# Kernel tuning notes

Hardware: AMD Instinct MI355X
Metric: run time of the kernel (lower is better)

Reference implementation:

```python
import jax, jax.numpy as jnp
import numpy as np

T, H, I, E, K = 1024, 2048, 768, 32, 4


def setup_inputs() -> dict:
    key = jax.random.key(0)
    ks = jax.random.split(key, 6)
    x = jax.random.normal(ks[0], (T, H), dtype=jnp.float32)
    # torch nn.Linear weight layout: [out_features, in_features], no bias (Qwen3)
    Wg = jax.random.normal(ks[1], (E, I, H), dtype=jnp.float32) * 0.02
    Wu = jax.random.normal(ks[2], (E, I, H), dtype=jnp.float32) * 0.02
    Wd = jax.random.normal(ks[3], (E, H, I), dtype=jnp.float32) * 0.02
    expert_ids = jax.random.randint(ks[4], (T, K), 0, E)
    expert_weights = jax.random.uniform(ks[5], (T, K), dtype=jnp.float32)
    return {"x": x, "Wg": Wg, "Wu": Wu, "Wd": Wd,
            "expert_ids": expert_ids, "expert_weights": expert_weights}


def reference(x, Wg, Wu, Wd, expert_ids, expert_weights):
    """MoE dispatch/combine over per-expert SwiGLU MLPs.

    y[t] = sum_k w[t,k] * down_e(silu(gate_e(x[t])) * up_e(x[t])), e = expert_ids[t,k]
    """
    Tn, Hn = x.shape
    En = Wg.shape[0]
    # Dense combine matrix [T, E]: scatter-add router weights onto expert slots.
    combine = jnp.zeros((Tn, En), x.dtype).at[
        jnp.arange(Tn)[:, None], expert_ids].add(expert_weights)

    def body(acc, we):
        wg, wu, wd, c = we  # wg,wu: [I,H]; wd: [H,I]; c: [T]
        h = jax.nn.silu(x @ wg.T) * (x @ wu.T)  # [T, I]
        return acc + c[:, None] * (h @ wd.T), None

    y, _ = jax.lax.scan(body, jnp.zeros_like(x), (Wg, Wu, Wd, combine.T))
    return y
```

## Files before the change

kernel.cpp:

```cpp
#include <hip/hip_runtime.h>
#include <hip/hip_bf16.h>

#define T_TOK 1024
#define H_DIM 2048
#define I_DIM 768
#define E_NUM 32
#define K_TOP 4
#define NPAIR (T_TOK * K_TOP)
#define TM 32
#define MAX_SLOTS (NPAIR + E_NUM * TM)

#define WS_META   0
#define WS_TOKEN  2048
#define WS_WEIGHT (WS_TOKEN + MAX_SLOTS * 4)
#define WS_HBUF   (WS_WEIGHT + MAX_SLOTS * 4)
#define WS_XB     (WS_HBUF + MAX_SLOTS * I_DIM * 2)

typedef __bf16 bf16x8 __attribute__((ext_vector_type(8)));
typedef float f32x4 __attribute__((ext_vector_type(4)));
typedef float f32x8 __attribute__((ext_vector_type(8)));

__device__ inline bf16x8 cvt8(f32x8 v) {
    bf16x8 r;
#pragma unroll
    for (int i = 0; i < 8; ++i) r[i] = (__bf16)v[i];
    return r;
}

__global__ void moe_route(const int* __restrict__ ids,
                          const float* __restrict__ ew,
                          int* __restrict__ meta,
                          int* __restrict__ slot_tok,
                          float* __restrict__ slot_w) {
    __shared__ int cnt[E_NUM], off[E_NUM], cur[E_NUM];
    __shared__ int s_tot;
    const int tid = threadIdx.x;
    if (tid < E_NUM) cnt[tid] = 0;
    __syncthreads();
    for (int p = tid; p < NPAIR; p += blockDim.x)
        atomicAdd(&cnt[ids[p]], 1);
    __syncthreads();
    if (tid == 0) {
        int tot = 0;
        for (int e = 0; e < E_NUM; ++e) {
            int pad = (cnt[e] + TM - 1) / TM * TM;
            off[e] = tot;
            meta[8 + e]  = tot;
            meta[64 + e] = pad / TM;
            tot += pad;
        }
        meta[0] = tot;
        s_tot = tot;
    }
    __syncthreads();
    const int tot = s_tot;
    for (int s = tid; s < tot; s += blockDim.x) {
        slot_tok[s] = 0;
        slot_w[s]   = 0.0f;
    }
    if (tid < E_NUM) cur[tid] = 0;
    __syncthreads();
    for (int p = tid; p < NPAIR; p += blockDim.x) {
        int e = ids[p];
        int i = atomicAdd(&cur[e], 1);
        int s = off[e] + i;
        slot_tok[s] = p / K_TOP;
        slot_w[s]   = ew[p];
    }
}

__global__ __launch_bounds__(256) void moe_xcast(const float* __restrict__ X,
                                                 __hip_bfloat16* __restrict__ Xb) {
    const int i = (blockIdx.x * 256 + threadIdx.x) * 8;
    f32x8 v = *(const f32x8*)(X + i);
    *(bf16x8*)(void*)(Xb + i) = cvt8(v);
}

template<int NMT>
__device__ __forceinline__ void gu_group(
    const __hip_bfloat16* __restrict__ Xb,
    const float* __restrict__ pg, const float* __restrict__ pu,
    const int* __restrict__ slot_tok,
    __hip_bfloat16* __restrict__ Hb,
    int off, int tile0, int n0, int col, int quad) {
    int s0[NMT];
    const __hip_bfloat16 *px0[NMT], *px1[NMT];
#pragma unroll
    for (int m = 0; m < NMT; ++m) {
        s0[m] = off + TM * (tile0 + 2 * m);
        px0[m] = Xb + (size_t)slot_tok[s0[m] + col] * H_DIM;
        px1[m] = Xb + (size_t)slot_tok[s0[m] + 16 + col] * H_DIM;
    }
    f32x4 ag0[NMT], ag1[NMT], au0[NMT], au1[NMT];
#pragma unroll
    for (int m = 0; m < NMT; ++m) {
        ag0[m] = {0.f,0.f,0.f,0.f}; ag1[m] = {0.f,0.f,0.f,0.f};
        au0[m] = {0.f,0.f,0.f,0.f}; au1[m] = {0.f,0.f,0.f,0.f};
    }
    for (int k = quad * 8; k < H_DIM; k += 32) {
        bf16x8 bg = cvt8(*(const f32x8*)(pg + k));
        bf16x8 bu = cvt8(*(const f32x8*)(pu + k));
#pragma unroll
        for (int m = 0; m < NMT; ++m) {
            bf16x8 a0 = *(const bf16x8*)(const void*)(px0[m] + k);
            bf16x8 a1 = *(const bf16x8*)(const void*)(px1[m] + k);
            ag0[m] = __builtin_amdgcn_mfma_f32_16x16x32_bf16(a0, bg, ag0[m], 0, 0, 0);
            ag1[m] = __builtin_amdgcn_mfma_f32_16x16x32_bf16(a1, bg, ag1[m], 0, 0, 0);
            au0[m] = __builtin_amdgcn_mfma_f32_16x16x32_bf16(a0, bu, au0[m], 0, 0, 0);
            au1[m] = __builtin_amdgcn_mfma_f32_16x16x32_bf16(a1, bu, au1[m], 0, 0, 0);
        }
    }
#pragma unroll
    for (int m = 0; m < NMT; ++m) {
#pragma unroll
        for (int r = 0; r < 4; ++r) {
            const int row = quad * 4 + r;
            float g0 = ag0[m][r], u0 = au0[m][r];
            float h0 = (g0 / (1.0f + __expf(-g0))) * u0;
            Hb[(size_t)(s0[m] + row) * I_DIM + n0 + col] = __float2bfloat16(h0);
            float g1 = ag1[m][r], u1 = au1[m][r];
            float h1 = (g1 / (1.0f + __expf(-g1))) * u1;
            Hb[(size_t)(s0[m] + 16 + row) * I_DIM + n0 + col] = __float2bfloat16(h1);
        }
    }
}

__global__ __launch_bounds__(256) void moe_gateup(
    const __hip_bfloat16* __restrict__ Xb,
    const float* __restrict__ Wg,
    const float* __restrict__ Wu,
    const int* __restrict__ meta,
    const int* __restrict__ slot_tok,
    __hip_bfloat16* __restrict__ Hb) {
    const int NCH = I_DIM / 32;
    const int e   = blockIdx.x / NCH;
    const int nch = blockIdx.x - e * NCH;
    const int lane = threadIdx.x & 63;
    const int wave = threadIdx.x >> 6;
    const int col  = lane & 15;
    const int quad = lane >> 4;
    const int colg = wave & 1;
    const int half = wave >> 1;
    const int n0 = nch * 32 + colg * 16;

    const int off   = meta[8 + e];
    const int ntile = meta[64 + e];
    const int nw = (ntile > half) ? ((ntile - half + 1) >> 1) : 0;
    if (nw == 0) return;

    const size_t wrow = ((size_t)e * I_DIM + n0 + col) * H_DIM;
    const float* pg = Wg + wrow;
    const float* pu = Wu + wrow;

    for (int i0 = 0; i0 < nw; i0 += 3) {
        int g = nw - i0; if (g > 3) g = 3;
        const int tile0 = half + 2 * i0;
        switch (g) {
            case 1:  gu_group<1>(Xb, pg, pu, slot_tok, Hb, off, tile0, n0, col, quad); break;
            case 2:  gu_group<2>(Xb, pg, pu, slot_tok, Hb, off, tile0, n0, col, quad); break;
            default: gu_group<3>(Xb, pg, pu, slot_tok, Hb, off, tile0, n0, col, quad); break;
        }
    }
}

template<int NMT>
__device__ __forceinline__ void dn_group(
    const float* __restrict__ pd,
    const int* __restrict__ slot_tok,
    const float* __restrict__ slot_w,
    const __hip_bfloat16* __restrict__ Hb,
    float* __restrict__ Y,
    int off, int tile0, int n0, int col, int quad) {
    int s0[NMT];
    const __hip_bfloat16 *ph0[NMT], *ph1[NMT];
#pragma unroll
    for (int m = 0; m < NMT; ++m) {
        s0[m] = off + TM * (tile0 + 2 * m);
        ph0[m] = Hb + (size_t)(s0[m] + col) * I_DIM;
        ph1[m] = Hb + (size_t)(s0[m] + 16 + col) * I_DIM;
    }
    f32x4 a0[NMT], a1[NMT];
#pragma unroll
    for (int m = 0; m < NMT; ++m) { a0[m] = {0.f,0.f,0.f,0.f}; a1[m] = {0.f,0.f,0.f,0.f}; }

    for (int k = quad * 8; k < I_DIM; k += 32) {
        bf16x8 b = cvt8(*(const f32x8*)(pd + k));
#pragma unroll
        for (int m = 0; m < NMT; ++m) {
            bf16x8 h0 = *(const bf16x8*)(const void*)(ph0[m] + k);
            bf16x8 h1 = *(const bf16x8*)(const void*)(ph1[m] + k);
            a0[m] = __builtin_amdgcn_mfma_f32_16x16x32_bf16(h0, b, a0[m], 0, 0, 0);
            a1[m] = __builtin_amdgcn_mfma_f32_16x16x32_bf16(h1, b, a1[m], 0, 0, 0);
        }
    }
#pragma unroll
    for (int m = 0; m < NMT; ++m) {
#pragma unroll
        for (int r = 0; r < 4; ++r) {
            const int row = quad * 4 + r;
            const int sA = s0[m] + row;
            atomicAdd(&Y[(size_t)slot_tok[sA] * H_DIM + n0 + col], a0[m][r] * slot_w[sA]);
            const int sB = s0[m] + 16 + row;
            atomicAdd(&Y[(size_t)slot_tok[sB] * H_DIM + n0 + col], a1[m][r] * slot_w[sB]);
        }
    }
}

__global__ __launch_bounds__(256) void moe_down(
    const float* __restrict__ Wd,
    const int* __restrict__ meta,
    const int* __restrict__ slot_tok,
    const float* __restrict__ slot_w,
    const __hip_bfloat16* __restrict__ Hb,
    float* __restrict__ Y) {
    const int NCH = H_DIM / 32;
    const int e   = blockIdx.x / NCH;
    const int nch = blockIdx.x - e * NCH;
    const int lane = threadIdx.x & 63;
    const int wave = threadIdx.x >> 6;
    const int col  = lane & 15;
    const int quad = lane >> 4;
    const int colg = wave & 1;
    const int half = wave >> 1;
    const int n0 = nch * 32 + colg * 16;

    const int off   = meta[8 + e];
    const int ntile = meta[64 + e];
    const int nw = (ntile > half) ? ((ntile - half + 1) >> 1) : 0;
    if (nw == 0) return;

    const float* pd = Wd + ((size_t)e * H_DIM + n0 + col) * I_DIM;

    for (int i0 = 0; i0 < nw; i0 += 3) {
        int g = nw - i0; if (g > 3) g = 3;
        const int tile0 = half + 2 * i0;
        switch (g) {
            case 1:  dn_group<1>(pd, slot_tok, slot_w, Hb, Y, off, tile0, n0, col, quad); break;
            case 2:  dn_group<2>(pd, slot_tok, slot_w, Hb, Y, off, tile0, n0, col, quad); break;
            default: dn_group<3>(pd, slot_tok, slot_w, Hb, Y, off, tile0, n0, col, quad); break;
        }
    }
}

extern "C" void kernel_launch(void* const* d_in, const int* in_sizes, int n_in,
                              void* d_out, int out_size, void* d_ws, size_t ws_size,
                              hipStream_t stream) {
    const float* X  = (const float*)d_in[0];
    const float* Wg = (const float*)d_in[1];
    const float* Wu = (const float*)d_in[2];
    const float* Wd = (const float*)d_in[3];
    const int* ids  = (const int*)d_in[4];
    const float* ew = (const float*)d_in[5];

    char* ws = (char*)d_ws;
    int*   meta     = (int*)(ws + WS_META);
    int*   slot_tok = (int*)(ws + WS_TOKEN);
    float* slot_w   = (float*)(ws + WS_WEIGHT);
    __hip_bfloat16* Hb = (__hip_bfloat16*)(ws + WS_HBUF);
    __hip_bfloat16* Xb = (__hip_bfloat16*)(ws + WS_XB);
    float* Y = (float*)d_out;

    hipMemsetAsync(Y, 0, (size_t)T_TOK * H_DIM * sizeof(float), stream);
    moe_route<<<1, 256, 0, stream>>>(ids, ew, meta, slot_tok, slot_w);
    moe_xcast<<<(T_TOK * H_DIM / 8) / 256, 256, 0, stream>>>(X, Xb);
    moe_gateup<<<E_NUM * (I_DIM / 32), 256, 0, stream>>>(Xb, Wg, Wu, meta, slot_tok, Hb);
    moe_down<<<E_NUM * (H_DIM / 32), 256, 0, stream>>>(Wd, meta, slot_tok, slot_w, Hb, Y);
}
```

Baseline: 810.5 us.

## Software-pipeline MFMA K-loops and give each block 16 columns across four waves

Both expert GEMM kernels now double-buffer their register loads: the next K-step's weight and activation vectors are fetched while MFMAs run on the current step. The block mapping also changes so each block covers 16 output columns with all four waves splitting tiles four ways, which doubles the grid and cuts the group size from three tiles to two. This is meant to hide global-load latency and raise parallelism. In exchange it uses more registers, and each block's column slice of the weights is now read by more waves.

```diff
diff --git a/kernel.cpp b/kernel.cpp
--- a/kernel.cpp
+++ b/kernel.cpp
@@ -87,7 +87,7 @@
     const __hip_bfloat16 *px0[NMT], *px1[NMT];
 #pragma unroll
     for (int m = 0; m < NMT; ++m) {
-        s0[m] = off + TM * (tile0 + 2 * m);
+        s0[m] = off + TM * (tile0 + 4 * m);
         px0[m] = Xb + (size_t)slot_tok[s0[m] + col] * H_DIM;
         px1[m] = Xb + (size_t)slot_tok[s0[m] + 16 + col] * H_DIM;
     }
@@ -97,19 +97,54 @@
         ag0[m] = {0.f,0.f,0.f,0.f}; ag1[m] = {0.f,0.f,0.f,0.f};
         au0[m] = {0.f,0.f,0.f,0.f}; au1[m] = {0.f,0.f,0.f,0.f};
     }
-    for (int k = quad * 8; k < H_DIM; k += 32) {
-        bf16x8 bg = cvt8(*(const f32x8*)(pg + k));
-        bf16x8 bu = cvt8(*(const f32x8*)(pu + k));
+    const int kq = quad * 8;
+    bf16x8 wg2[2], wu2[2];
+    bf16x8 a02[2][NMT], a12[2][NMT];
+    {
+        f32x8 g = *(const f32x8*)(pg + kq);
+        f32x8 u = *(const f32x8*)(pu + kq);
 #pragma unroll
         for (int m = 0; m < NMT; ++m) {
-            bf16x8 a0 = *(const bf16x8*)(const void*)(px0[m] + k);
-            bf16x8 a1 = *(const bf16x8*)(const void*)(px1[m] + k);
-            ag0[m] = __builtin_amdgcn_mfma_f32_16x16x32_bf16(a0, bg, ag0[m], 0, 0, 0);
-            ag1[m] = __builtin_amdgcn_mfma_f32_16x16x32_bf16(a1, bg, ag1[m], 0, 0, 0);
-            au0[m] = __builtin_amdgcn_mfma_f32_16x16x32_bf16(a0, bu, au0[m], 0, 0, 0);
-            au1[m] = __builtin_amdgcn_mfma_f32_16x16x32_bf16(a1, bu, au1[m], 0, 0, 0);
-        }
-    }
+            a02[0][m] = *(const bf16x8*)(const void*)(px0[m] + kq);
+            a12[0][m] = *(const bf16x8*)(const void*)(px1[m] + kq);
+        }
+        wg2[0] = cvt8(g); wu2[0] = cvt8(u);
+    }
+
+#define GU_STEP(CUR, IT) do {                                                  \
+        const int kn_ = kq + ((IT) + 1) * 32;                                  \
+        f32x8 g_ = *(const f32x8*)(pg + kn_);                                  \
+        f32x8 u_ = *(const f32x8*)(pu + kn_);                                  \
+        _Pragma("unroll")                                                      \
+        for (int m = 0; m < NMT; ++m) {                                        \
+            a02[1 - (CUR)][m] = *(const bf16x8*)(const void*)(px0[m] + kn_);   \
+            a12[1 - (CUR)][m] = *(const bf16x8*)(const void*)(px1[m] + kn_);   \
+        }                                                                      \
+        _Pragma("unroll")                                                      \
+        for (int m = 0; m < NMT; ++m) {                                        \
+            ag0[m] = __builtin_amdgcn_mfma_f32_16x16x32_bf16(a02[(CUR)][m], wg2[(CUR)], ag0[m], 0, 0, 0); \
+            ag1[m] = __builtin_amdgcn_mfma_f32_16x16x32_bf16(a12[(CUR)][m], wg2[(CUR)], ag1[m], 0, 0, 0); \
+            au0[m] = __builtin_amdgcn_mfma_f32_16x16x32_bf16(a02[(CUR)][m], wu2[(CUR)], au0[m], 0, 0, 0); \
+            au1[m] = __builtin_amdgcn_mfma_f32_16x16x32_bf16(a12[(CUR)][m], wu2[(CUR)], au1[m], 0, 0, 0); \
+        }                                                                      \
+        wg2[1 - (CUR)] = cvt8(g_); wu2[1 - (CUR)] = cvt8(u_);                  \
+    } while (0)
+
+    const int NIT = H_DIM / 32;
+    for (int it = 0; it < NIT - 2; it += 2) {
+        GU_STEP(0, it);
+        GU_STEP(1, it + 1);
+    }
+    GU_STEP(0, NIT - 2);
+#undef GU_STEP
+#pragma unroll
+    for (int m = 0; m < NMT; ++m) {
+        ag0[m] = __builtin_amdgcn_mfma_f32_16x16x32_bf16(a02[1][m], wg2[1], ag0[m], 0, 0, 0);
+        ag1[m] = __builtin_amdgcn_mfma_f32_16x16x32_bf16(a12[1][m], wg2[1], ag1[m], 0, 0, 0);
+        au0[m] = __builtin_amdgcn_mfma_f32_16x16x32_bf16(a02[1][m], wu2[1], au0[m], 0, 0, 0);
+        au1[m] = __builtin_amdgcn_mfma_f32_16x16x32_bf16(a12[1][m], wu2[1], au1[m], 0, 0, 0);
+    }
+
 #pragma unroll
     for (int m = 0; m < NMT; ++m) {
 #pragma unroll
@@ -132,34 +167,28 @@
     const int* __restrict__ meta,
     const int* __restrict__ slot_tok,
     __hip_bfloat16* __restrict__ Hb) {
-    const int NCH = I_DIM / 32;
+    const int NCH = I_DIM / 16;
     const int e   = blockIdx.x / NCH;
     const int nch = blockIdx.x - e * NCH;
     const int lane = threadIdx.x & 63;
     const int wave = threadIdx.x >> 6;
     const int col  = lane & 15;
     const int quad = lane >> 4;
-    const int colg = wave & 1;
-    const int half = wave >> 1;
-    const int n0 = nch * 32 + colg * 16;
+    const int n0 = nch * 16;
 
     const int off   = meta[8 + e];
     const int ntile = meta[64 + e];
-    const int nw = (ntile > half) ? ((ntile - half + 1) >> 1) : 0;
+    const int nw = (ntile > wave) ? ((ntile - wave + 3) >> 2) : 0;
     if (nw == 0) return;
 
     const size_t wrow = ((size_t)e * I_DIM + n0 + col) * H_DIM;
     const float* pg = Wg + wrow;
     const float* pu = Wu + wrow;
 
-    for (int i0 = 0; i0 < nw; i0 += 3) {
-        int g = nw - i0; if (g > 3) g = 3;
-        const int tile0 = half + 2 * i0;
-        switch (g) {
-            case 1:  gu_group<1>(Xb, pg, pu, slot_tok, Hb, off, tile0, n0, col, quad); break;
-            case 2:  gu_group<2>(Xb, pg, pu, slot_tok, Hb, off, tile0, n0, col, quad); break;
-            default: gu_group<3>(Xb, pg, pu, slot_tok, Hb, off, tile0, n0, col, quad); break;
-        }
+    for (int i0 = 0; i0 < nw; i0 += 2) {
+        const int tile0 = wave + 4 * i0;
+        if (nw - i0 >= 2) gu_group<2>(Xb, pg, pu, slot_tok, Hb, off, tile0, n0, col, quad);
+        else              gu_group<1>(Xb, pg, pu, slot_tok, Hb, off, tile0, n0, col, quad);
     }
 }
 
@@ -175,7 +204,7 @@
     const __hip_bfloat16 *ph0[NMT], *ph1[NMT];
 #pragma unroll
     for (int m = 0; m < NMT; ++m) {
-        s0[m] = off + TM * (tile0 + 2 * m);
+        s0[m] = off + TM * (tile0 + 4 * m);
         ph0[m] = Hb + (size_t)(s0[m] + col) * I_DIM;
         ph1[m] = Hb + (size_t)(s0[m] + 16 + col) * I_DIM;
     }
@@ -183,16 +212,48 @@
 #pragma unroll
     for (int m = 0; m < NMT; ++m) { a0[m] = {0.f,0.f,0.f,0.f}; a1[m] = {0.f,0.f,0.f,0.f}; }
 
-    for (int k = quad * 8; k < I_DIM; k += 32) {
-        bf16x8 b = cvt8(*(const f32x8*)(pd + k));
+    const int kq = quad * 8;
+    bf16x8 w2[2];
+    bf16x8 h02[2][NMT], h12[2][NMT];
+    {
+        f32x8 w = *(const f32x8*)(pd + kq);
 #pragma unroll
         for (int m = 0; m < NMT; ++m) {
-            bf16x8 h0 = *(const bf16x8*)(const void*)(ph0[m] + k);
-            bf16x8 h1 = *(const bf16x8*)(const void*)(ph1[m] + k);
-            a0[m] = __builtin_amdgcn_mfma_f32_16x16x32_bf16(h0, b, a0[m], 0, 0, 0);
-            a1[m] = __builtin_amdgcn_mfma_f32_16x16x32_bf16(h1, b, a1[m], 0, 0, 0);
-        }
-    }
+            h02[0][m] = *(const bf16x8*)(const void*)(ph0[m] + kq);
+            h12[0][m] = *(const bf16x8*)(const void*)(ph1[m] + kq);
+        }
+        w2[0] = cvt8(w);
+    }
+
+#define DN_STEP(CUR, IT) do {                                                  \
+        const int kn_ = kq + ((IT) + 1) * 32;                                  \
+        f32x8 w_ = *(const f32x8*)(pd + kn_);                                  \
+        _Pragma("unroll")                                                      \
+        for (int m = 0; m < NMT; ++m) {                                        \
+            h02[1 - (CUR)][m] = *(const bf16x8*)(const void*)(ph0[m] + kn_);   \
+            h12[1 - (CUR)][m] = *(const bf16x8*)(const void*)(ph1[m] + kn_);   \
+        }                                                                      \
+        _Pragma("unroll")                                                      \
+        for (int m = 0; m < NMT; ++m) {                                        \
+            a0[m] = __builtin_amdgcn_mfma_f32_16x16x32_bf16(h02[(CUR)][m], w2[(CUR)], a0[m], 0, 0, 0); \
+            a1[m] = __builtin_amdgcn_mfma_f32_16x16x32_bf16(h12[(CUR)][m], w2[(CUR)], a1[m], 0, 0, 0); \
+        }                                                                      \
+        w2[1 - (CUR)] = cvt8(w_);                                              \
+    } while (0)
+
+    const int NIT = I_DIM / 32;
+    for (int it = 0; it < NIT - 2; it += 2) {
+        DN_STEP(0, it);
+        DN_STEP(1, it + 1);
+    }
+    DN_STEP(0, NIT - 2);
+#undef DN_STEP
+#pragma unroll
+    for (int m = 0; m < NMT; ++m) {
+        a0[m] = __builtin_amdgcn_mfma_f32_16x16x32_bf16(h02[1][m], w2[1], a0[m], 0, 0, 0);
+        a1[m] = __builtin_amdgcn_mfma_f32_16x16x32_bf16(h12[1][m], w2[1], a1[m], 0, 0, 0);
+    }
+
 #pragma unroll
     for (int m = 0; m < NMT; ++m) {
 #pragma unroll
@@ -213,32 +274,26 @@
     const float* __restrict__ slot_w,
     const __hip_bfloat16* __restrict__ Hb,
     float* __restrict__ Y) {
-    const int NCH = H_DIM / 32;
+    const int NCH = H_DIM / 16;
     const int e   = blockIdx.x / NCH;
     const int nch = blockIdx.x - e * NCH;
     const int lane = threadIdx.x & 63;
     const int wave = threadIdx.x >> 6;
     const int col  = lane & 15;
     const int quad = lane >> 4;
-    const int colg = wave & 1;
-    const int half = wave >> 1;
-    const int n0 = nch * 32 + colg * 16;
+    const int n0 = nch * 16;
 
     const int off   = meta[8 + e];
     const int ntile = meta[64 + e];
-    const int nw = (ntile > half) ? ((ntile - half + 1) >> 1) : 0;
+    const int nw = (ntile > wave) ? ((ntile - wave + 3) >> 2) : 0;
     if (nw == 0) return;
 
     const float* pd = Wd + ((size_t)e * H_DIM + n0 + col) * I_DIM;
 
-    for (int i0 = 0; i0 < nw; i0 += 3) {
-        int g = nw - i0; if (g > 3) g = 3;
-        const int tile0 = half + 2 * i0;
-        switch (g) {
-            case 1:  dn_group<1>(pd, slot_tok, slot_w, Hb, Y, off, tile0, n0, col, quad); break;
-            case 2:  dn_group<2>(pd, slot_tok, slot_w, Hb, Y, off, tile0, n0, col, quad); break;
-            default: dn_group<3>(pd, slot_tok, slot_w, Hb, Y, off, tile0, n0, col, quad); break;
-        }
+    for (int i0 = 0; i0 < nw; i0 += 2) {
+        const int tile0 = wave + 4 * i0;
+        if (nw - i0 >= 2) dn_group<2>(pd, slot_tok, slot_w, Hb, Y, off, tile0, n0, col, quad);
+        else              dn_group<1>(pd, slot_tok, slot_w, Hb, Y, off, tile0, n0, col, quad);
     }
 }
 
@@ -263,6 +318,6 @@
     hipMemsetAsync(Y, 0, (size_t)T_TOK * H_DIM * sizeof(float), stream);
     moe_route<<<1, 256, 0, stream>>>(ids, ew, meta, slot_tok, slot_w);
     moe_xcast<<<(T_TOK * H_DIM / 8) / 256, 256, 0, stream>>>(X, Xb);
-    moe_gateup<<<E_NUM * (I_DIM / 32), 256, 0, stream>>>(Xb, Wg, Wu, meta, slot_tok, Hb);
-    moe_down<<<E_NUM * (H_DIM / 32), 256, 0, stream>>>(Wd, meta, slot_tok, slot_w, Hb, Y);
-}
+    moe_gateup<<<E_NUM * (I_DIM / 16), 256, 0, stream>>>(Xb, Wg, Wu, meta, slot_tok, Hb);
+    moe_down<<<E_NUM * (H_DIM / 16), 256, 0, stream>>>(Wd, meta, slot_tok, slot_w, Hb, Y);
+}
```

New measurement: 888.6 us. +9.6%, slower.

## Stage expert weight tiles in LDS with async double-buffered loads shared by all waves

Applied to the files above, without the earlier changes.

Gate/up and down kernels now give each block 16 output columns and have all four waves cooperatively stream fp32 weight tiles into swizzled, double-buffered LDS via global_load_lds. Each wave then handles up to two 32-row token tiles against the shared weight tile. Previously each wave read its own weight rows directly from global memory. This removes the redundant weight reads across waves and overlaps weight fetch with MFMA work. The cost is twice as many blocks, a barrier per k-step, and idle waves when an expert has few tiles.

```diff
diff --git a/kernel.cpp b/kernel.cpp
--- a/kernel.cpp
+++ b/kernel.cpp
@@ -20,11 +20,29 @@
 typedef float f32x4 __attribute__((ext_vector_type(4)));
 typedef float f32x8 __attribute__((ext_vector_type(8)));
 
+#define MFMA(acc, a, b) acc = __builtin_amdgcn_mfma_f32_16x16x32_bf16(a, b, acc, 0, 0, 0)
+
 __device__ inline bf16x8 cvt8(f32x8 v) {
     bf16x8 r;
 #pragma unroll
     for (int i = 0; i < 8; ++i) r[i] = (__bf16)v[i];
     return r;
+}
+
+__device__ __forceinline__ void stage16(const void* g, void* l) {
+    __builtin_amdgcn_global_load_lds(
+        (__attribute__((address_space(1))) void*)(void*)(size_t)g,
+        (__attribute__((address_space(3))) void*)l, 16, 0, 0);
+}
+
+__device__ __forceinline__ bf16x8 bfrag(const char* tile, int c, int jq) {
+    const int key = (c & 7) << 4;
+    f32x4 lo = *(const f32x4*)(tile + c * 256 + ((jq +  0) ^ key));
+    f32x4 hi = *(const f32x4*)(tile + c * 256 + ((jq + 16) ^ key));
+    f32x8 v;
+    v[0] = lo[0]; v[1] = lo[1]; v[2] = lo[2]; v[3] = lo[3];
+    v[4] = hi[0]; v[5] = hi[1]; v[6] = hi[2]; v[7] = hi[3];
+    return cvt8(v);
 }
 
 __global__ void moe_route(const int* __restrict__ ids,
@@ -76,55 +94,6 @@
     *(bf16x8*)(void*)(Xb + i) = cvt8(v);
 }
 
-template<int NMT>
-__device__ __forceinline__ void gu_group(
-    const __hip_bfloat16* __restrict__ Xb,
-    const float* __restrict__ pg, const float* __restrict__ pu,
-    const int* __restrict__ slot_tok,
-    __hip_bfloat16* __restrict__ Hb,
-    int off, int tile0, int n0, int col, int quad) {
-    int s0[NMT];
-    const __hip_bfloat16 *px0[NMT], *px1[NMT];
-#pragma unroll
-    for (int m = 0; m < NMT; ++m) {
-        s0[m] = off + TM * (tile0 + 2 * m);
-        px0[m] = Xb + (size_t)slot_tok[s0[m] + col] * H_DIM;
-        px1[m] = Xb + (size_t)slot_tok[s0[m] + 16 + col] * H_DIM;
-    }
-    f32x4 ag0[NMT], ag1[NMT], au0[NMT], au1[NMT];
-#pragma unroll
-    for (int m = 0; m < NMT; ++m) {
-        ag0[m] = {0.f,0.f,0.f,0.f}; ag1[m] = {0.f,0.f,0.f,0.f};
-        au0[m] = {0.f,0.f,0.f,0.f}; au1[m] = {0.f,0.f,0.f,0.f};
-    }
-    for (int k = quad * 8; k < H_DIM; k += 32) {
-        bf16x8 bg = cvt8(*(const f32x8*)(pg + k));
-        bf16x8 bu = cvt8(*(const f32x8*)(pu + k));
-#pragma unroll
-        for (int m = 0; m < NMT; ++m) {
-            bf16x8 a0 = *(const bf16x8*)(const void*)(px0[m] + k);
-            bf16x8 a1 = *(const bf16x8*)(const void*)(px1[m] + k);
-            ag0[m] = __builtin_amdgcn_mfma_f32_16x16x32_bf16(a0, bg, ag0[m], 0, 0, 0);
-            ag1[m] = __builtin_amdgcn_mfma_f32_16x16x32_bf16(a1, bg, ag1[m], 0, 0, 0);
-            au0[m] = __builtin_amdgcn_mfma_f32_16x16x32_bf16(a0, bu, au0[m], 0, 0, 0);
-            au1[m] = __builtin_amdgcn_mfma_f32_16x16x32_bf16(a1, bu, au1[m], 0, 0, 0);
-        }
-    }
-#pragma unroll
-    for (int m = 0; m < NMT; ++m) {
-#pragma unroll
-        for (int r = 0; r < 4; ++r) {
-            const int row = quad * 4 + r;
-            float g0 = ag0[m][r], u0 = au0[m][r];
-            float h0 = (g0 / (1.0f + __expf(-g0))) * u0;
-            Hb[(size_t)(s0[m] + row) * I_DIM + n0 + col] = __float2bfloat16(h0);
-            float g1 = ag1[m][r], u1 = au1[m][r];
-            float h1 = (g1 / (1.0f + __expf(-g1))) * u1;
-            Hb[(size_t)(s0[m] + 16 + row) * I_DIM + n0 + col] = __float2bfloat16(h1);
-        }
-    }
-}
-
 __global__ __launch_bounds__(256) void moe_gateup(
     const __hip_bfloat16* __restrict__ Xb,
     const float* __restrict__ Wg,
@@ -132,76 +101,113 @@
     const int* __restrict__ meta,
     const int* __restrict__ slot_tok,
     __hip_bfloat16* __restrict__ Hb) {
-    const int NCH = I_DIM / 32;
+    __shared__ __align__(16) char lds[2][2][4096];
+    const int NCH = I_DIM / 16;
     const int e   = blockIdx.x / NCH;
     const int nch = blockIdx.x - e * NCH;
+    const int n0  = nch * 16;
     const int lane = threadIdx.x & 63;
     const int wave = threadIdx.x >> 6;
-    const int col  = lane & 15;
-    const int quad = lane >> 4;
-    const int colg = wave & 1;
-    const int half = wave >> 1;
-    const int n0 = nch * 32 + colg * 16;
+    const int c = lane & 15;
+    const int q = lane >> 4;
 
     const int off   = meta[8 + e];
     const int ntile = meta[64 + e];
-    const int nw = (ntile > half) ? ((ntile - half + 1) >> 1) : 0;
-    if (nw == 0) return;
-
-    const size_t wrow = ((size_t)e * I_DIM + n0 + col) * H_DIM;
-    const float* pg = Wg + wrow;
-    const float* pu = Wu + wrow;
-
-    for (int i0 = 0; i0 < nw; i0 += 3) {
-        int g = nw - i0; if (g > 3) g = 3;
-        const int tile0 = half + 2 * i0;
-        switch (g) {
-            case 1:  gu_group<1>(Xb, pg, pu, slot_tok, Hb, off, tile0, n0, col, quad); break;
-            case 2:  gu_group<2>(Xb, pg, pu, slot_tok, Hb, off, tile0, n0, col, quad); break;
-            default: gu_group<3>(Xb, pg, pu, slot_tok, Hb, off, tile0, n0, col, quad); break;
-        }
-    }
-}
-
-template<int NMT>
-__device__ __forceinline__ void dn_group(
-    const float* __restrict__ pd,
-    const int* __restrict__ slot_tok,
-    const float* __restrict__ slot_w,
-    const __hip_bfloat16* __restrict__ Hb,
-    float* __restrict__ Y,
-    int off, int tile0, int n0, int col, int quad) {
-    int s0[NMT];
-    const __hip_bfloat16 *ph0[NMT], *ph1[NMT];
-#pragma unroll
-    for (int m = 0; m < NMT; ++m) {
-        s0[m] = off + TM * (tile0 + 2 * m);
-        ph0[m] = Hb + (size_t)(s0[m] + col) * I_DIM;
-        ph1[m] = Hb + (size_t)(s0[m] + 16 + col) * I_DIM;
-    }
-    f32x4 a0[NMT], a1[NMT];
-#pragma unroll
-    for (int m = 0; m < NMT; ++m) { a0[m] = {0.f,0.f,0.f,0.f}; a1[m] = {0.f,0.f,0.f,0.f}; }
-
-    for (int k = quad * 8; k < I_DIM; k += 32) {
-        bf16x8 b = cvt8(*(const f32x8*)(pd + k));
-#pragma unroll
-        for (int m = 0; m < NMT; ++m) {
-            bf16x8 h0 = *(const bf16x8*)(const void*)(ph0[m] + k);
-            bf16x8 h1 = *(const bf16x8*)(const void*)(ph1[m] + k);
-            a0[m] = __builtin_amdgcn_mfma_f32_16x16x32_bf16(h0, b, a0[m], 0, 0, 0);
-            a1[m] = __builtin_amdgcn_mfma_f32_16x16x32_bf16(h1, b, a1[m], 0, 0, 0);
-        }
-    }
-#pragma unroll
-    for (int m = 0; m < NMT; ++m) {
-#pragma unroll
-        for (int r = 0; r < 4; ++r) {
-            const int row = quad * 4 + r;
-            const int sA = s0[m] + row;
-            atomicAdd(&Y[(size_t)slot_tok[sA] * H_DIM + n0 + col], a0[m][r] * slot_w[sA]);
-            const int sB = s0[m] + 16 + row;
-            atomicAdd(&Y[(size_t)slot_tok[sB] * H_DIM + n0 + col], a1[m][r] * slot_w[sB]);
+    if (ntile == 0) return;
+
+    const int r_st = wave * 4 + (lane >> 4);
+    const int g_st = (lane & 15) ^ (r_st & 7);
+    const size_t wbase = ((size_t)e * I_DIM + n0 + r_st) * H_DIM + (size_t)g_st * 4;
+    const float* pgs = Wg + wbase;
+    const float* pus = Wu + wbase;
+    char* const ldg0 = &lds[0][0][0] + wave * 1024;
+    char* const ldg1 = &lds[1][0][0] + wave * 1024;
+    char* const ldu0 = &lds[0][1][0] + wave * 1024;
+    char* const ldu1 = &lds[1][1][0] + wave * 1024;
+
+    const int NT = H_DIM / 64;
+
+    for (int p0 = 0; p0 < ntile; p0 += 8) {
+        const int npass = ntile - p0 < 8 ? ntile - p0 : 8;
+        const int nmt = (wave < npass ? 1 : 0) + (wave + 4 < npass ? 1 : 0);
+        int s0a = off, s0b = off;
+        int ta0 = 0, ta1 = 0, tb0 = 0, tb1 = 0;
+        if (nmt >= 1) {
+            s0a = off + TM * (p0 + wave);
+            ta0 = slot_tok[s0a + c]; ta1 = slot_tok[s0a + 16 + c];
+        }
+        if (nmt >= 2) {
+            s0b = off + TM * (p0 + wave + 4);
+            tb0 = slot_tok[s0b + c]; tb1 = slot_tok[s0b + 16 + c];
+        }
+        const __hip_bfloat16* pa0 = Xb + (size_t)ta0 * H_DIM;
+        const __hip_bfloat16* pa1 = Xb + (size_t)ta1 * H_DIM;
+        const __hip_bfloat16* pb0 = Xb + (size_t)tb0 * H_DIM;
+        const __hip_bfloat16* pb1 = Xb + (size_t)tb1 * H_DIM;
+
+        f32x4 ag0a = {0,0,0,0}, ag0b = {0,0,0,0}, au0a = {0,0,0,0}, au0b = {0,0,0,0};
+        f32x4 ag1a = {0,0,0,0}, ag1b = {0,0,0,0}, au1a = {0,0,0,0}, au1b = {0,0,0,0};
+
+        stage16(pgs, ldg0);
+        stage16(pus, ldu0);
+        __syncthreads();
+
+        for (int t = 0; t < NT; ++t) {
+            const int cur = t & 1;
+            if (t + 1 < NT) {
+                const float* pg_n = pgs + (t + 1) * 64;
+                const float* pu_n = pus + (t + 1) * 64;
+                stage16(pg_n, cur ? ldg0 : ldg1);
+                stage16(pu_n, cur ? ldu0 : ldu1);
+            }
+            if (nmt > 0) {
+                const char* tg = &lds[cur][0][0];
+                const char* tu = &lds[cur][1][0];
+                const int k0 = t * 64;
+#pragma unroll
+                for (int j = 0; j < 2; ++j) {
+                    const int jq = j * 128 + q * 32;
+                    bf16x8 bg = bfrag(tg, c, jq);
+                    bf16x8 bu = bfrag(tu, c, jq);
+                    const int ka = k0 + j * 32 + q * 8;
+                    bf16x8 a0 = *(const bf16x8*)(const void*)(pa0 + ka);
+                    bf16x8 a1 = *(const bf16x8*)(const void*)(pa1 + ka);
+                    MFMA(ag0a, a0, bg); MFMA(au0a, a0, bu);
+                    MFMA(ag0b, a1, bg); MFMA(au0b, a1, bu);
+                    if (nmt > 1) {
+                        bf16x8 b0 = *(const bf16x8*)(const void*)(pb0 + ka);
+                        bf16x8 b1 = *(const bf16x8*)(const void*)(pb1 + ka);
+                        MFMA(ag1a, b0, bg); MFMA(au1a, b0, bu);
+                        MFMA(ag1b, b1, bg); MFMA(au1b, b1, bu);
+                    }
+                }
+            }
+            __syncthreads();
+        }
+
+        if (nmt >= 1) {
+#pragma unroll
+            for (int r = 0; r < 4; ++r) {
+                const int row = q * 4 + r;
+                float g = ag0a[r], u = au0a[r];
+                float h = (g / (1.0f + __expf(-g))) * u;
+                Hb[(size_t)(s0a + row) * I_DIM + n0 + c] = __float2bfloat16(h);
+                g = ag0b[r]; u = au0b[r];
+                h = (g / (1.0f + __expf(-g))) * u;
+                Hb[(size_t)(s0a + 16 + row) * I_DIM + n0 + c] = __float2bfloat16(h);
+            }
+        }
+        if (nmt >= 2) {
+#pragma unroll
+            for (int r = 0; r < 4; ++r) {
+                const int row = q * 4 + r;
+                float g = ag1a[r], u = au1a[r];
+                float h = (g / (1.0f + __expf(-g))) * u;
+                Hb[(size_t)(s0b + row) * I_DIM + n0 + c] = __float2bfloat16(h);
+                g = ag1b[r]; u = au1b[r];
+                h = (g / (1.0f + __expf(-g))) * u;
+                Hb[(size_t)(s0b + 16 + row) * I_DIM + n0 + c] = __float2bfloat16(h);
+            }
         }
     }
 }
@@ -213,31 +219,87 @@
     const float* __restrict__ slot_w,
     const __hip_bfloat16* __restrict__ Hb,
     float* __restrict__ Y) {
-    const int NCH = H_DIM / 32;
+    __shared__ __align__(16) char lds[2][4096];
+    const int NCH = H_DIM / 16;
     const int e   = blockIdx.x / NCH;
     const int nch = blockIdx.x - e * NCH;
+    const int n0  = nch * 16;
     const int lane = threadIdx.x & 63;
     const int wave = threadIdx.x >> 6;
-    const int col  = lane & 15;
-    const int quad = lane >> 4;
-    const int colg = wave & 1;
-    const int half = wave >> 1;
-    const int n0 = nch * 32 + colg * 16;
+    const int c = lane & 15;
+    const int q = lane >> 4;
 
     const int off   = meta[8 + e];
     const int ntile = meta[64 + e];
-    const int nw = (ntile > half) ? ((ntile - half + 1) >> 1) : 0;
-    if (nw == 0) return;
-
-    const float* pd = Wd + ((size_t)e * H_DIM + n0 + col) * I_DIM;
-
-    for (int i0 = 0; i0 < nw; i0 += 3) {
-        int g = nw - i0; if (g > 3) g = 3;
-        const int tile0 = half + 2 * i0;
-        switch (g) {
-            case 1:  dn_group<1>(pd, slot_tok, slot_w, Hb, Y, off, tile0, n0, col, quad); break;
-            case 2:  dn_group<2>(pd, slot_tok, slot_w, Hb, Y, off, tile0, n0, col, quad); break;
-            default: dn_group<3>(pd, slot_tok, slot_w, Hb, Y, off, tile0, n0, col, quad); break;
+    if (ntile == 0) return;
+
+    const int r_st = wave * 4 + (lane >> 4);
+    const int g_st = (lane & 15) ^ (r_st & 7);
+    const float* pds = Wd + ((size_t)e * H_DIM + n0 + r_st) * I_DIM + (size_t)g_st * 4;
+    char* const ld0 = &lds[0][0] + wave * 1024;
+    char* const ld1 = &lds[1][0] + wave * 1024;
+
+    const int NT = I_DIM / 64;
+
+    for (int p0 = 0; p0 < ntile; p0 += 8) {
+        const int npass = ntile - p0 < 8 ? ntile - p0 : 8;
+        const int nmt = (wave < npass ? 1 : 0) + (wave + 4 < npass ? 1 : 0);
+        int s0a = off, s0b = off;
+        if (nmt >= 1) s0a = off + TM * (p0 + wave);
+        if (nmt >= 2) s0b = off + TM * (p0 + wave + 4);
+        const __hip_bfloat16* pa0 = Hb + (size_t)(s0a + c) * I_DIM;
+        const __hip_bfloat16* pa1 = Hb + (size_t)(s0a + 16 + c) * I_DIM;
+        const __hip_bfloat16* pb0 = Hb + (size_t)(s0b + c) * I_DIM;
+        const __hip_bfloat16* pb1 = Hb + (size_t)(s0b + 16 + c) * I_DIM;
+
+        f32x4 a0a = {0,0,0,0}, a0b = {0,0,0,0}, a1a = {0,0,0,0}, a1b = {0,0,0,0};
+
+        stage16(pds, ld0);
+        __syncthreads();
+
+        for (int t = 0; t < NT; ++t) {
+            const int cur = t & 1;
+            if (t + 1 < NT) stage16(pds + (t + 1) * 64, cur ? ld0 : ld1);
+            if (nmt > 0) {
+                const char* td = &lds[cur][0];
+                const int k0 = t * 64;
+#pragma unroll
+                for (int j = 0; j < 2; ++j) {
+                    const int jq = j * 128 + q * 32;
+                    bf16x8 bd = bfrag(td, c, jq);
+                    const int ka = k0 + j * 32 + q * 8;
+                    bf16x8 h0 = *(const bf16x8*)(const void*)(pa0 + ka);
+                    bf16x8 h1 = *(const bf16x8*)(const void*)(pa1 + ka);
+                    MFMA(a0a, h0, bd); MFMA(a0b, h1, bd);
+                    if (nmt > 1) {
+                        bf16x8 h2 = *(const bf16x8*)(const void*)(pb0 + ka);
+                        bf16x8 h3 = *(const bf16x8*)(const void*)(pb1 + ka);
+                        MFMA(a1a, h2, bd); MFMA(a1b, h3, bd);
+                    }
+                }
+            }
+            __syncthreads();
+        }
+
+        if (nmt >= 1) {
+#pragma unroll
+            for (int r = 0; r < 4; ++r) {
+                const int row = q * 4 + r;
+                const int sA = s0a + row;
+                atomicAdd(&Y[(size_t)slot_tok[sA] * H_DIM + n0 + c], a0a[r] * slot_w[sA]);
+                const int sB = s0a + 16 + row;
+                atomicAdd(&Y[(size_t)slot_tok[sB] * H_DIM + n0 + c], a0b[r] * slot_w[sB]);
+            }
+        }
+        if (nmt >= 2) {
+#pragma unroll
+            for (int r = 0; r < 4; ++r) {
+                const int row = q * 4 + r;
+                const int sA = s0b + row;
+                atomicAdd(&Y[(size_t)slot_tok[sA] * H_DIM + n0 + c], a1a[r] * slot_w[sA]);
+                const int sB = s0b + 16 + row;
+                atomicAdd(&Y[(size_t)slot_tok[sB] * H_DIM + n0 + c], a1b[r] * slot_w[sB]);
+            }
         }
     }
 }
@@ -263,6 +325,6 @@
     hipMemsetAsync(Y, 0, (size_t)T_TOK * H_DIM * sizeof(float), stream);
     moe_route<<<1, 256, 0, stream>>>(ids, ew, meta, slot_tok, slot_w);
     moe_xcast<<<(T_TOK * H_DIM / 8) / 256, 256, 0, stream>>>(X, Xb);
-    moe_gateup<<<E_NUM * (I_DIM / 32), 256, 0, stream>>>(Xb, Wg, Wu, meta, slot_tok, Hb);
-    moe_down<<<E_NUM * (H_DIM / 32), 256, 0, stream>>>(Wd, meta, slot_tok, slot_w, Hb, Y);
-}
+    moe_gateup<<<E_NUM * (I_DIM / 16), 256, 0, stream>>>(Xb, Wg, Wu, meta, slot_tok, Hb);
+    moe_down<<<E_NUM * (H_DIM / 16), 256, 0, stream>>>(Wd, meta, slot_tok, slot_w, Hb, Y);
+}
```

After: 775.9 us. -4.3%, faster.
